# Performance work log

Measured on AMD Instinct MI355X. Metric: run time of the kernel, lower is better.

Reference implementation:

```python
import jax, jax.numpy as jnp
import numpy as np

E = 256

def setup_inputs() -> dict:
    key = jax.random.key(0)
    ks = jax.random.split(key, 10)
    N, T_y, T_x = 8, 300, 160
    s = 1.0 / np.sqrt(E)  # torch-style uniform-ish init scale, keeps gates unsaturated
    return {
        "inputs": jax.random.normal(ks[0], (N, T_y, E // 2), jnp.float32),
        "memory": jax.random.normal(ks[1], (N, T_x, E), jnp.float32),
        "h0": jnp.zeros((1, N, E), jnp.float32),
        "Wih": jax.random.normal(ks[2], (3 * E, E // 2), jnp.float32) * s,
        "Whh": jax.random.normal(ks[3], (3 * E, E), jnp.float32) * s,
        "bih": jax.random.normal(ks[4], (3 * E,), jnp.float32) * s,
        "bhh": jax.random.normal(ks[5], (3 * E,), jnp.float32) * s,
        "W": jax.random.normal(ks[6], (E, E), jnp.float32) * s,
        "U": jax.random.normal(ks[7], (E, E), jnp.float32) * s,
        "v": jax.random.normal(ks[8], (E,), jnp.float32) * s,
    }


def reference(inputs, memory, h0, Wih, Whh, bih, bhh, W, U, v):
    # GRU (PyTorch gate order r, z, n), batch_first, single layer, unidirectional.
    def step(h, x_t):
        gi = x_t @ Wih.T + bih      # [N, 3E]
        gh = h @ Whh.T + bhh        # [N, 3E]
        ir, iz, i_n = jnp.split(gi, 3, axis=-1)
        hr, hz, hn = jnp.split(gh, 3, axis=-1)
        r = jax.nn.sigmoid(ir + hr)
        z = jax.nn.sigmoid(iz + hz)
        n = jnp.tanh(i_n + r * hn)
        h_new = (1.0 - z) * n + z * h
        return h_new, h_new

    h_last, outs = jax.lax.scan(step, h0[0], jnp.swapaxes(inputs, 0, 1))
    outputs = jnp.swapaxes(outs, 0, 1)   # [N, T_y, E]
    hidden = h_last[None]                # [1, N, E]

    # Bahdanau additive attention
    w = outputs @ W.T                    # [N, T_y, E]
    u = memory @ U.T                     # [N, T_x, E]
    # scores: v . tanh(w + u) broadcast over [N, T_y, T_x, E]
    scores = jnp.einsum('ntxe,e->ntx', jnp.tanh(w[:, :, None, :] + u[:, None, :, :]), v)
    attn_weights = jax.nn.softmax(scores, axis=2)  # [N, T_y, T_x]
    return attn_weights, outputs, hidden
```

## Files before the change

### kernel.cpp

```cpp
#include <hip/hip_runtime.h>


typedef _Float16 f16x2 __attribute__((ext_vector_type(2)));
typedef _Float16 f16x8 __attribute__((ext_vector_type(8)));
typedef float f32x4 __attribute__((ext_vector_type(4)));

__device__ __forceinline__ float fexp2(float x) { return __builtin_amdgcn_exp2f(x); }
__device__ __forceinline__ float frcp(float x) { return __builtin_amdgcn_rcpf(x); }
__device__ __forceinline__ float fsig(float x) {
    return frcp(1.0f + fexp2(x * -1.4426950408889634f));
}
__device__ __forceinline__ float ftanh(float x) {
    return 1.0f - 2.0f * frcp(1.0f + fexp2(x * 2.8853900817779268f));
}

__device__ __forceinline__ float pick4(f32x4 v, int s) {
    float ab = (s & 1) ? v[1] : v[0];
    float cd = (s & 1) ? v[3] : v[2];
    return (s & 2) ? cd : ab;
}

#define FLAG(i) ((i) * 32)

__global__ __launch_bounds__(256) void phase1_kernel(
    const float* __restrict__ Whh, unsigned* __restrict__ wd,
    const float* __restrict__ inputs, const float* __restrict__ Wih,
    float* __restrict__ gi, const float* __restrict__ bih,
    const float* __restrict__ bhh) {
    if (blockIdx.x < 384) {
        int gid = blockIdx.x * 256 + threadIdx.x;
        int i = gid >> 9, t = gid & 511;
        int fi = i >> 2, j = i & 3;
        int g = fi >> 4, m2 = (fi >> 3) & 1, ks = fi & 7;
        int w = t >> 6, l = t & 63;
        int row = 256 * g + 32 * w + 16 * m2 + (l & 15);
        int k = 32 * ks + 8 * (l >> 4) + 2 * j;
        union { unsigned u; f16x2 h; } cv;
        cv.h[0] = (_Float16)Whh[(size_t)row * 256 + k];
        cv.h[1] = (_Float16)Whh[(size_t)row * 256 + k + 1];
        wd[i * 512 + t] = cv.u;
        return;
    }
    int id = blockIdx.x - 384;
    const int n0 = (id % 12) * 64, m0 = (id / 12) * 64;
    __shared__ float Xs[32][65];
    __shared__ float Ws2[32][65];
    const int tid = threadIdx.x;
    const int tx = tid & 15, ty = tid >> 4;
    const int M = 2400, K = 128;
    float acc[4][4] = {};
    for (int k0 = 0; k0 < K; k0 += 32) {
#pragma unroll
        for (int i = 0; i < 8; ++i) {
            int e = tid + i * 256;
            int kk = e & 31, m = e >> 5;
            int row = m0 + m;
            Xs[kk][m] = (row < M) ? inputs[(size_t)row * K + k0 + kk] : 0.0f;
            Ws2[kk][m] = Wih[(size_t)(n0 + m) * K + k0 + kk];
        }
        __syncthreads();
#pragma unroll
        for (int kk = 0; kk < 32; ++kk) {
            float a[4], b[4];
#pragma unroll
            for (int i = 0; i < 4; ++i) a[i] = Xs[kk][ty * 4 + i];
#pragma unroll
            for (int j = 0; j < 4; ++j) b[j] = Ws2[kk][tx * 4 + j];
#pragma unroll
            for (int i = 0; i < 4; ++i)
#pragma unroll
                for (int j = 0; j < 4; ++j) acc[i][j] += a[i] * b[j];
        }
        __syncthreads();
    }
#pragma unroll
    for (int i = 0; i < 4; ++i) {
        int row = m0 + ty * 4 + i;
        if (row >= M) continue;
        int b = row / 300;
        int t = row - b * 300;
#pragma unroll
        for (int j = 0; j < 4; ++j) {
            int col = n0 + tx * 4 + j;
            float val = acc[i][j] + ((col < 512) ? (bih[col] + bhh[col]) : bih[col]);
            gi[(size_t)(t * 8 + b) * 768 + col] = val;
        }
    }
}

__global__ __launch_bounds__(256) void gemm_kernel(
    const float* __restrict__ X, const float* __restrict__ Wt,
    float* __restrict__ C, _Float16* __restrict__ C16,
    int M, int N, int K, int mode) {
    __shared__ float Xs[32][65];
    __shared__ float Ws2[32][65];
    const int n0 = blockIdx.x * 64, m0 = blockIdx.y * 64;
    const int tid = threadIdx.x;
    const int tx = tid & 15, ty = tid >> 4;
    float acc[4][4] = {};
    for (int k0 = 0; k0 < K; k0 += 32) {
#pragma unroll
        for (int i = 0; i < 8; ++i) {
            int e = tid + i * 256;
            int kk = e & 31, m = e >> 5;
            int row = m0 + m;
            Xs[kk][m] = (row < M) ? X[(size_t)row * K + k0 + kk] : 0.0f;
            Ws2[kk][m] = Wt[(size_t)(n0 + m) * K + k0 + kk];
        }
        __syncthreads();
#pragma unroll
        for (int kk = 0; kk < 32; ++kk) {
            float a[4], b[4];
#pragma unroll
            for (int i = 0; i < 4; ++i) a[i] = Xs[kk][ty * 4 + i];
#pragma unroll
            for (int j = 0; j < 4; ++j) b[j] = Ws2[kk][tx * 4 + j];
#pragma unroll
            for (int i = 0; i < 4; ++i)
#pragma unroll
                for (int j = 0; j < 4; ++j) acc[i][j] += a[i] * b[j];
        }
        __syncthreads();
    }
#pragma unroll
    for (int i = 0; i < 4; ++i) {
        int row = m0 + ty * 4 + i;
        if (row >= M) continue;
#pragma unroll
        for (int j = 0; j < 4; ++j) {
            int col = n0 + tx * 4 + j;
            if (mode == 2) C16[(size_t)row * N + col] = (_Float16)acc[i][j];
            else           C[(size_t)row * N + col] = acc[i][j];
        }
    }
}

__global__ __launch_bounds__(512, 1) void gru_mega(
    float* __restrict__ gi, unsigned* __restrict__ wd,
    const float* __restrict__ h0, const float* __restrict__ bhh,
    float* __restrict__ outs, float* __restrict__ hid,
    const float* __restrict__ memory, const float* __restrict__ Um,
    _Float16* __restrict__ u16, const float* __restrict__ W,
    const float* __restrict__ vv, float* __restrict__ attn,
    const float* __restrict__ Whh, const float* __restrict__ inputs,
    const float* __restrict__ Wih, const float* __restrict__ bih,
    int* flags, int full) {
    __shared__ __align__(16) _Float16 hbuf[2][256];
    __shared__ float Xs[32][65];
    __shared__ float Ws2[32][65];
    __shared__ unsigned uS[160 * 129];
    __shared__ __align__(16) float oL[10][260];
    __shared__ float wLf[10][256];
    __shared__ float vL[256];
    __shared__ float scP[2][2][160];
    __shared__ float sc2[2][160];
    __shared__ float red2[2][2];

    const int tid = threadIdx.x;

    if (full) {
        for (int task = blockIdx.x; task < 840; task += 248) {
            if (task < 384) {
                if (tid < 256) {
                    int gid = task * 256 + tid;
                    int i = gid >> 9, t = gid & 511;
                    int fi = i >> 2, j = i & 3;
                    int g = fi >> 4, m2 = (fi >> 3) & 1, ks = fi & 7;
                    int w = t >> 6, l = t & 63;
                    int row = 256 * g + 32 * w + 16 * m2 + (l & 15);
                    int k = 32 * ks + 8 * (l >> 4) + 2 * j;
                    union { unsigned u; f16x2 h; } cv;
                    cv.h[0] = (_Float16)Whh[(size_t)row * 256 + k];
                    cv.h[1] = (_Float16)Whh[(size_t)row * 256 + k + 1];
                    wd[i * 512 + t] = cv.u;
                }
            } else {
                int tt = task - 384;
                const int n0 = (tt % 12) * 64, m0 = (tt / 12) * 64;
                const int tx = tid & 15, ty = tid >> 4;
                float acc[2][4] = {};
                for (int k0 = 0; k0 < 128; k0 += 32) {
#pragma unroll
                    for (int i = 0; i < 4; ++i) {
                        int e = tid + i * 512;
                        int kk = e & 31, m = e >> 5;
                        int row = m0 + m;
                        Xs[kk][m] = (row < 2400)
                                        ? inputs[(size_t)row * 128 + k0 + kk]
                                        : 0.0f;
                        Ws2[kk][m] = Wih[(size_t)(n0 + m) * 128 + k0 + kk];
                    }
                    __syncthreads();
#pragma unroll
                    for (int kk = 0; kk < 32; ++kk) {
                        float a0 = Xs[kk][ty * 2], a1 = Xs[kk][ty * 2 + 1];
                        float b0 = Ws2[kk][tx * 4 + 0];
                        float b1 = Ws2[kk][tx * 4 + 1];
                        float b2 = Ws2[kk][tx * 4 + 2];
                        float b3 = Ws2[kk][tx * 4 + 3];
                        acc[0][0] += a0 * b0; acc[0][1] += a0 * b1;
                        acc[0][2] += a0 * b2; acc[0][3] += a0 * b3;
                        acc[1][0] += a1 * b0; acc[1][1] += a1 * b1;
                        acc[1][2] += a1 * b2; acc[1][3] += a1 * b3;
                    }
                    __syncthreads();
                }
#pragma unroll
                for (int i = 0; i < 2; ++i) {
                    int row = m0 + ty * 2 + i;
                    if (row < 2400) {
                        int bb = row / 300;
                        int t2 = row - bb * 300;
#pragma unroll
                        for (int j = 0; j < 4; ++j) {
                            int col = n0 + tx * 4 + j;
                            float val = acc[i][j] +
                                ((col < 512) ? (bih[col] + bhh[col]) : bih[col]);
                            gi[(size_t)(t2 * 8 + bb) * 768 + col] = val;
                        }
                    }
                }
            }
            __syncthreads();
        }
        asm volatile("s_waitcnt vmcnt(0)" ::: "memory");
        __syncthreads();
        if (tid == 0) {
            __hip_atomic_fetch_add(&flags[FLAG(9)], 1, __ATOMIC_RELEASE,
                                   __HIP_MEMORY_SCOPE_AGENT);
            while (__hip_atomic_load(&flags[FLAG(9)], __ATOMIC_ACQUIRE,
                                     __HIP_MEMORY_SCOPE_AGENT) < 248)
                __builtin_amdgcn_s_sleep(16);
        }
        __syncthreads();
    }

    if (blockIdx.x >= 8) {
        int id = blockIdx.x - 8;
        if (id < 80) {
            const int n0 = (id & 3) * 64, m0 = (id >> 2) * 64;
            const int tx = tid & 15, ty = (tid & 255) >> 4;
            float acc[4][4] = {};
            for (int k0 = 0; k0 < 256; k0 += 32) {
                if (tid < 256) {
#pragma unroll
                    for (int i = 0; i < 8; ++i) {
                        int e = tid + i * 256;
                        int kk = e & 31, m = e >> 5;
                        Xs[kk][m] = memory[(size_t)(m0 + m) * 256 + k0 + kk];
                        Ws2[kk][m] = Um[(size_t)(n0 + m) * 256 + k0 + kk];
                    }
                }
                __syncthreads();
                if (tid < 256) {
#pragma unroll
                    for (int kk = 0; kk < 32; ++kk) {
                        float a[4], b[4];
#pragma unroll
                        for (int i = 0; i < 4; ++i) a[i] = Xs[kk][ty * 4 + i];
#pragma unroll
                        for (int j = 0; j < 4; ++j) b[j] = Ws2[kk][tx * 4 + j];
#pragma unroll
                        for (int i = 0; i < 4; ++i)
#pragma unroll
                            for (int j = 0; j < 4; ++j) acc[i][j] += a[i] * b[j];
                    }
                }
                __syncthreads();
            }
            if (tid < 256) {
#pragma unroll
                for (int i = 0; i < 4; ++i)
#pragma unroll
                    for (int j = 0; j < 4; ++j)
                        u16[(size_t)(m0 + ty * 4 + i) * 256 + n0 + tx * 4 + j] =
                            (_Float16)acc[i][j];
            }
            if (!full) return;
            __syncthreads();
            if (tid == 0)
                __hip_atomic_fetch_add(&flags[FLAG(8)], 1, __ATOMIC_RELEASE,
                                       __HIP_MEMORY_SCOPE_AGENT);
        }
        if (!full) return;

        const int grp = id / 30;
        const int tc = id % 30;
        if (tid == 0) {
            while (__hip_atomic_load(&flags[FLAG(8)], __ATOMIC_RELAXED,
                                     __HIP_MEMORY_SCOPE_AGENT) < 80)
                __builtin_amdgcn_s_sleep(64);
            while (__hip_atomic_load(&flags[FLAG(8)], __ATOMIC_ACQUIRE,
                                     __HIP_MEMORY_SCOPE_AGENT) < 80)
                __builtin_amdgcn_s_sleep(8);
        }
        __syncthreads();
        const unsigned* ug = (const unsigned*)(u16 + (size_t)grp * 160 * 256);
        for (int i = tid; i < 20480; i += 512)
            uS[(i >> 7) * 129 + (i & 127)] = ug[i];
        if (tid < 256) vL[tid] = vv[tid];
        __syncthreads();

        if (tid == 0) {
            while (__hip_atomic_load(&flags[FLAG(grp)], __ATOMIC_RELAXED,
                                     __HIP_MEMORY_SCOPE_AGENT) < 1)
                __builtin_amdgcn_s_sleep(127);
            while (__hip_atomic_load(&flags[FLAG(grp)], __ATOMIC_ACQUIRE,
                                     __HIP_MEMORY_SCOPE_AGENT) < 1)
                __builtin_amdgcn_s_sleep(8);
        }
        __syncthreads();
        for (int i = tid; i < 2560; i += 512) {
            int ti = i >> 8, k = i & 255;
            oL[ti][k] = outs[((size_t)grp * 300 + tc * 10 + ti) * 256 + k];
        }
        __syncthreads();
        {
            const int c = tid & 255, rh = tid >> 8;
            float a0 = 0, a1 = 0, a2 = 0, a3 = 0, a4 = 0;
            const float* wr = W + (size_t)c * 256;
            const int r0 = rh * 5;
            for (int k4 = 0; k4 < 256; k4 += 4) {
                float4 wq = *(const float4*)(wr + k4);
#define WROW(ACC, TI)                                                     \
                {                                                         \
                    float4 oq = *(const float4*)(&oL[TI][k4]);            \
                    ACC += wq.x * oq.x + wq.y * oq.y +                    \
                           wq.z * oq.z + wq.w * oq.w;                     \
                }
                WROW(a0, r0 + 0) WROW(a1, r0 + 1) WROW(a2, r0 + 2)
                WROW(a3, r0 + 3) WROW(a4, r0 + 4)
#undef WROW
            }
            wLf[r0 + 0][c] = a0; wLf[r0 + 1][c] = a1; wLf[r0 + 2][c] = a2;
            wLf[r0 + 3][c] = a3; wLf[r0 + 4][c] = a4;
        }
        __syncthreads();
        for (int tp = 0; tp < 5; ++tp) {
            const int ti0 = tp * 2;
            if (tid < 320) {
                const int x = (tid < 160) ? tid : tid - 160;
                const int half = (tid >= 160) ? 1 : 0;
                const unsigned* ur = uS + x * 129 + half * 64;
                const float* wl0 = wLf[ti0] + half * 128;
                const float* wl1 = wLf[ti0 + 1] + half * 128;
                const float* vl = vL + half * 128;
                float a0 = 0.f, b0 = 0.f, a1 = 0.f, b1 = 0.f;
#pragma unroll 8
                for (int e2 = 0; e2 < 64; ++e2) {
                    union { unsigned uu2; _Float16 hh[2]; } cv;
                    cv.uu2 = ur[e2];
                    int ee = e2 * 2;
                    float u0 = (float)cv.hh[0], u1 = (float)cv.hh[1];
                    float v0 = vl[ee], v1 = vl[ee + 1];
                    a0 += v0 * ftanh(wl0[ee] + u0);
                    b0 += v1 * ftanh(wl0[ee + 1] + u1);
                    a1 += v0 * ftanh(wl1[ee] + u0);
                    b1 += v1 * ftanh(wl1[ee + 1] + u1);
                }
                scP[0][half][x] = a0 + b0;
                scP[1][half][x] = a1 + b1;
            }
            __syncthreads();
            if (tid < 320) {
                int r = (tid >= 160) ? 1 : 0;
                int x = r ? tid - 160 : tid;
                sc2[r][x] = scP[r][0][x] + scP[r][1][x];
            }
            __syncthreads();
            if (tid < 128) {
                int r = tid >> 6, lane = tid & 63;
                float m = -3.0e38f;
                for (int i = lane; i < 160; i += 64) m = fmaxf(m, sc2[r][i]);
#pragma unroll
                for (int o = 32; o; o >>= 1) m = fmaxf(m, __shfl_xor(m, o));
                if (lane == 0) red2[r][0] = m;
            }
            __syncthreads();
            if (tid < 320) {
                int r = (tid >= 160) ? 1 : 0;
                int x = r ? tid - 160 : tid;
                sc2[r][x] = fexp2((sc2[r][x] - red2[r][0]) *
                                  1.4426950408889634f);
            }
            __syncthreads();
            if (tid < 128) {
                int r = tid >> 6, lane = tid & 63;
                float s = 0.0f;
                for (int i = lane; i < 160; i += 64) s += sc2[r][i];
#pragma unroll
                for (int o = 32; o; o >>= 1) s += __shfl_xor(s, o);
                if (lane == 0) red2[r][1] = s;
            }
            __syncthreads();
            if (tid < 320) {
                int r = (tid >= 160) ? 1 : 0;
                int x = r ? tid - 160 : tid;
                attn[(size_t)(grp * 300 + tc * 10 + ti0 + r) * 160 + x] =
                    sc2[r][x] * frcp(red2[r][1]);
            }
            __syncthreads();
        }
        return;
    }

    const int b = blockIdx.x;
    const int t = tid;
    const int w = t >> 6, l = t & 63;
    const int grp = l >> 4;
    const int sel = l & 7;
    const int hi = (l >> 3) & 1;
    const int m2s = sel >> 2, rsel = sel & 3;
    const int e = 32 * w + 16 * m2s + 4 * grp + rsel;

    f16x8 wf[48];
#pragma unroll
    for (int fi = 0; fi < 48; ++fi) {
        union { unsigned u[4]; f16x8 v; } cv;
#pragma unroll
        for (int j = 0; j < 4; ++j) cv.u[j] = wd[(fi * 4 + j) * 512 + t];
        wf[fi] = cv.v;
    }

    float h = h0[b * 256 + e];
    float bn = bhh[512 + e];
    if (!hi) hbuf[0][e] = (_Float16)h;
    const float* gp = gi + b * 768;
    float* op = outs + (size_t)b * 76800 + e;

    float gr = gp[e], gz = gp[e + 256], gn = gp[e + 512];
    __syncthreads();

    for (int st = 0; st < 300; ++st) {
        int stn = (st < 299) ? st + 1 : st;
        const float* g = gp + (size_t)stn * 6144;
        float grn = g[e], gzn = g[e + 256], gnn = g[e + 512];

        const _Float16* hb = hbuf[st & 1];
        f16x8 hv0 = *(const f16x8*)(hb + 0 * 32 + 8 * grp);
        f16x8 hv1 = *(const f16x8*)(hb + 1 * 32 + 8 * grp);
        f16x8 hv2 = *(const f16x8*)(hb + 2 * 32 + 8 * grp);
        f16x8 hv3 = *(const f16x8*)(hb + 3 * 32 + 8 * grp);
        f16x8 hv4 = *(const f16x8*)(hb + 4 * 32 + 8 * grp);
        f16x8 hv5 = *(const f16x8*)(hb + 5 * 32 + 8 * grp);
        f16x8 hv6 = *(const f16x8*)(hb + 6 * 32 + 8 * grp);
        f16x8 hv7 = *(const f16x8*)(hb + 7 * 32 + 8 * grp);

        f32x4 aR0 = {0.f, 0.f, 0.f, 0.f}, aR1 = {0.f, 0.f, 0.f, 0.f};
        f32x4 aZ0 = {0.f, 0.f, 0.f, 0.f}, aZ1 = {0.f, 0.f, 0.f, 0.f};
        f32x4 aN0 = {0.f, 0.f, 0.f, 0.f}, aN1 = {0.f, 0.f, 0.f, 0.f};
#define KSTEP(ks, hv)                                                        \
        aR0 = __builtin_amdgcn_mfma_f32_16x16x32_f16(wf[0 * 8 + ks], hv, aR0, 0, 0, 0); \
        aR1 = __builtin_amdgcn_mfma_f32_16x16x32_f16(wf[1 * 8 + ks], hv, aR1, 0, 0, 0); \
        aZ0 = __builtin_amdgcn_mfma_f32_16x16x32_f16(wf[2 * 8 + ks], hv, aZ0, 0, 0, 0); \
        aZ1 = __builtin_amdgcn_mfma_f32_16x16x32_f16(wf[3 * 8 + ks], hv, aZ1, 0, 0, 0); \
        aN0 = __builtin_amdgcn_mfma_f32_16x16x32_f16(wf[4 * 8 + ks], hv, aN0, 0, 0, 0); \
        aN1 = __builtin_amdgcn_mfma_f32_16x16x32_f16(wf[5 * 8 + ks], hv, aN1, 0, 0, 0);
        KSTEP(0, hv0) KSTEP(1, hv1) KSTEP(2, hv2) KSTEP(3, hv3)
        KSTEP(4, hv4) KSTEP(5, hv5) KSTEP(6, hv6) KSTEP(7, hv7)
#undef KSTEP

        f32x4 vR = m2s ? aR1 : aR0;
        f32x4 vZ = m2s ? aZ1 : aZ0;
        f32x4 vN = m2s ? aN1 : aN0;
        float sr = pick4(vR, rsel);
        float sz = pick4(vZ, rsel);
        float sn = pick4(vN, rsel);

        float r = fsig(gr + sr);
        float z = fsig(gz + sz);
        float n = ftanh(gn + r * (sn + bn));
        h = n + z * (h - n);

        gr = grn; gz = gzn; gn = gnn;

        if (hi)
            op[st * 256] = h;
        else
            hbuf[(st + 1) & 1][e] = (_Float16)h;
        asm volatile("s_waitcnt lgkmcnt(0)\n\ts_barrier" ::: "memory");
    }
    if (!hi) hid[b * 256 + e] = h;
    if (full) {
        asm volatile("s_waitcnt vmcnt(0)" ::: "memory");
        __syncthreads();
        if (t == 0)
            __hip_atomic_store(&flags[FLAG(b)], 1, __ATOMIC_RELEASE,
                               __HIP_MEMORY_SCOPE_AGENT);
    }
}

__global__ __launch_bounds__(256) void wattn_kernel(
    const _Float16* __restrict__ u16, const float* __restrict__ outs,
    const float* __restrict__ W, const float* __restrict__ vv,
    float* __restrict__ attn) {
    const int tc = blockIdx.x, b = blockIdx.y;
    const int tid = threadIdx.x;
    __shared__ unsigned uS[160 * 129];
    __shared__ __align__(16) float oL[10][260];
    __shared__ float wLf[10][256];
    __shared__ float vL[256], sc[160], red[2];

    const unsigned* ug = (const unsigned*)(u16 + (size_t)b * 160 * 256);
    for (int i = tid; i < 20480; i += 256)
        uS[(i >> 7) * 129 + (i & 127)] = ug[i];
    vL[tid] = vv[tid];
    for (int i = tid; i < 2560; i += 256) {
        int ti = i >> 8, k = i & 255;
        oL[ti][k] = outs[((size_t)b * 300 + tc * 10 + ti) * 256 + k];
    }
    __syncthreads();
    {
        float a0 = 0, a1 = 0, a2 = 0, a3 = 0, a4 = 0;
        float a5 = 0, a6 = 0, a7 = 0, a8 = 0, a9 = 0;
        for (int k4 = 0; k4 < 256; k4 += 4) {
            float4 wq = *(const float4*)(W + (size_t)tid * 256 + k4);
#define WROW(ACC, TI)                                                     \
            {                                                             \
                float4 oq = *(const float4*)(&oL[TI][k4]);                \
                ACC += wq.x * oq.x + wq.y * oq.y +                        \
                       wq.z * oq.z + wq.w * oq.w;                        \
            }
            WROW(a0, 0) WROW(a1, 1) WROW(a2, 2) WROW(a3, 3) WROW(a4, 4)
            WROW(a5, 5) WROW(a6, 6) WROW(a7, 7) WROW(a8, 8) WROW(a9, 9)
#undef WROW
        }
        wLf[0][tid] = a0; wLf[1][tid] = a1; wLf[2][tid] = a2;
        wLf[3][tid] = a3; wLf[4][tid] = a4; wLf[5][tid] = a5;
        wLf[6][tid] = a6; wLf[7][tid] = a7; wLf[8][tid] = a8;
        wLf[9][tid] = a9;
    }
    __syncthreads();
    for (int ti = 0; ti < 10; ++ti) {
        int t = tc * 10 + ti;
        float acc2 = 0.0f;
        if (tid < 160) {
            const unsigned* ur = uS + tid * 129;
            const float* wl = wLf[ti];
#pragma unroll 8
            for (int e2 = 0; e2 < 128; ++e2) {
                union { unsigned uu2; _Float16 hh[2]; } cv;
                cv.uu2 = ur[e2];
                int ee = e2 * 2;
                acc2 += vL[ee] * ftanh(wl[ee] + (float)cv.hh[0]);
                acc2 += vL[ee + 1] * ftanh(wl[ee + 1] + (float)cv.hh[1]);
            }
            sc[tid] = acc2;
        }
        __syncthreads();
        if (tid < 64) {
            float m = -3.0e38f;
            for (int i = tid; i < 160; i += 64) m = fmaxf(m, sc[i]);
#pragma unroll
            for (int o = 32; o; o >>= 1) m = fmaxf(m, __shfl_xor(m, o));
            if (tid == 0) red[0] = m;
        }
        __syncthreads();
        float ee = 0.0f;
        if (tid < 160) {
            ee = fexp2((acc2 - red[0]) * 1.4426950408889634f);
            sc[tid] = ee;
        }
        __syncthreads();
        if (tid < 64) {
            float s = 0.0f;
            for (int i = tid; i < 160; i += 64) s += sc[i];
#pragma unroll
            for (int o = 32; o; o >>= 1) s += __shfl_xor(s, o);
            if (tid == 0) red[1] = s;
        }
        __syncthreads();
        if (tid < 160)
            attn[(size_t)(b * 300 + t) * 160 + tid] = ee * frcp(red[1]);
        __syncthreads();
    }
}

extern "C" void kernel_launch(void* const* d_in, const int* in_sizes, int n_in,
                              void* d_out, int out_size, void* d_ws, size_t ws_size,
                              hipStream_t stream) {
    const float* inputs = (const float*)d_in[0];
    const float* memory = (const float*)d_in[1];
    const float* h0 = (const float*)d_in[2];
    const float* Wih = (const float*)d_in[3];
    const float* Whh = (const float*)d_in[4];
    const float* bih = (const float*)d_in[5];
    const float* bhh = (const float*)d_in[6];
    const float* Wm = (const float*)d_in[7];
    const float* Um = (const float*)d_in[8];
    const float* vv = (const float*)d_in[9];

    float* out = (float*)d_out;
    float* out_attn = out;
    float* out_outputs = out + 384000;
    float* out_hidden = out + 998400;

    char* ws = (char*)d_ws;
    float* gi = (float*)ws;
    unsigned* wd = (unsigned*)(ws + 7372800);

    const size_t U16_OFF = 7766016, FLAG_OFF = 8421376;
    const bool full = ws_size >= FLAG_OFF + 1280;
    _Float16* u16 = full ? (_Float16*)(ws + U16_OFF) : (_Float16*)ws;
    int* flags = (int*)(ws + FLAG_OFF);

    if (full) {
        hipMemsetAsync(flags, 0, 1280, stream);
        gru_mega<<<248, 512, 0, stream>>>(gi, wd, h0, bhh, out_outputs,
                                          out_hidden, memory, Um, u16, Wm, vv,
                                          out_attn, Whh, inputs, Wih, bih,
                                          flags, 1);
    } else {
        phase1_kernel<<<840, 256, 0, stream>>>(Whh, wd, inputs, Wih, gi, bih,
                                               bhh);
        gru_mega<<<8, 512, 0, stream>>>(gi, wd, h0, bhh, out_outputs,
                                        out_hidden, memory, Um, u16, Wm, vv,
                                        out_attn, Whh, inputs, Wih, bih,
                                        flags, 0);
        gemm_kernel<<<dim3(4, 20), 256, 0, stream>>>(memory, Um, nullptr, u16,
                                                     1280, 256, 256, 2);
        wattn_kernel<<<dim3(30, 8), 256, 0, stream>>>(u16, out_outputs, Wm, vv,
                                                      out_attn);
    }
}
```

Before: 484.1 us.

## Replace grid-wide barrier with one-way flag so GRU blocks alone wait for precompute

The 8 recurrence blocks no longer take part in the precompute work. The grid-wide barrier is replaced: the other 240 blocks signal a counter, and only the GRU blocks wait on it before loading weights. The other blocks can then go straight on to the memory@U.T GEMM without waiting for everyone. The input-projection GEMM tile grows from a 2x4 to a 4x4 microtile per thread, computed by 256 threads. Flag polling is split into a relaxed system-scope peek followed by one acquire load, and some sleep intervals are changed. This risks memory-ordering subtleties from mixing system and agent scopes.

```diff
diff --git a/kernel.cpp b/kernel.cpp
--- a/kernel.cpp
+++ b/kernel.cpp
@@ -21,6 +21,13 @@
 }
 
 #define FLAG(i) ((i) * 32)
+
+__device__ __forceinline__ int flag_peek(int* p) {
+    return __hip_atomic_load(p, __ATOMIC_RELAXED, __HIP_MEMORY_SCOPE_SYSTEM);
+}
+__device__ __forceinline__ void flag_fence(int* p) {
+    (void)__hip_atomic_load(p, __ATOMIC_ACQUIRE, __HIP_MEMORY_SCOPE_AGENT);
+}
 
 __global__ __launch_bounds__(256) void phase1_kernel(
     const float* __restrict__ Whh, unsigned* __restrict__ wd,
@@ -158,85 +165,88 @@
 
     const int tid = threadIdx.x;
 
-    if (full) {
-        for (int task = blockIdx.x; task < 840; task += 248) {
-            if (task < 384) {
-                if (tid < 256) {
-                    int gid = task * 256 + tid;
-                    int i = gid >> 9, t = gid & 511;
-                    int fi = i >> 2, j = i & 3;
-                    int g = fi >> 4, m2 = (fi >> 3) & 1, ks = fi & 7;
-                    int w = t >> 6, l = t & 63;
-                    int row = 256 * g + 32 * w + 16 * m2 + (l & 15);
-                    int k = 32 * ks + 8 * (l >> 4) + 2 * j;
-                    union { unsigned u; f16x2 h; } cv;
-                    cv.h[0] = (_Float16)Whh[(size_t)row * 256 + k];
-                    cv.h[1] = (_Float16)Whh[(size_t)row * 256 + k + 1];
-                    wd[i * 512 + t] = cv.u;
-                }
-            } else {
-                int tt = task - 384;
-                const int n0 = (tt % 12) * 64, m0 = (tt / 12) * 64;
-                const int tx = tid & 15, ty = tid >> 4;
-                float acc[2][4] = {};
-                for (int k0 = 0; k0 < 128; k0 += 32) {
-#pragma unroll
-                    for (int i = 0; i < 4; ++i) {
-                        int e = tid + i * 512;
-                        int kk = e & 31, m = e >> 5;
-                        int row = m0 + m;
-                        Xs[kk][m] = (row < 2400)
-                                        ? inputs[(size_t)row * 128 + k0 + kk]
-                                        : 0.0f;
-                        Ws2[kk][m] = Wih[(size_t)(n0 + m) * 128 + k0 + kk];
+    if (blockIdx.x >= 8) {
+        int id = blockIdx.x - 8;
+        if (full) {
+            for (int task = id; task < 840; task += 240) {
+                if (task < 384) {
+                    if (tid < 256) {
+                        int gid = task * 256 + tid;
+                        int i = gid >> 9, t = gid & 511;
+                        int fi = i >> 2, j = i & 3;
+                        int g = fi >> 4, m2 = (fi >> 3) & 1, ks = fi & 7;
+                        int w = t >> 6, l = t & 63;
+                        int row = 256 * g + 32 * w + 16 * m2 + (l & 15);
+                        int k = 32 * ks + 8 * (l >> 4) + 2 * j;
+                        union { unsigned u; f16x2 h; } cv;
+                        cv.h[0] = (_Float16)Whh[(size_t)row * 256 + k];
+                        cv.h[1] = (_Float16)Whh[(size_t)row * 256 + k + 1];
+                        wd[i * 512 + t] = cv.u;
                     }
-                    __syncthreads();
-#pragma unroll
-                    for (int kk = 0; kk < 32; ++kk) {
-                        float a0 = Xs[kk][ty * 2], a1 = Xs[kk][ty * 2 + 1];
-                        float b0 = Ws2[kk][tx * 4 + 0];
-                        float b1 = Ws2[kk][tx * 4 + 1];
-                        float b2 = Ws2[kk][tx * 4 + 2];
-                        float b3 = Ws2[kk][tx * 4 + 3];
-                        acc[0][0] += a0 * b0; acc[0][1] += a0 * b1;
-                        acc[0][2] += a0 * b2; acc[0][3] += a0 * b3;
-                        acc[1][0] += a1 * b0; acc[1][1] += a1 * b1;
-                        acc[1][2] += a1 * b2; acc[1][3] += a1 * b3;
+                } else {
+                    int tt = task - 384;
+                    const int n0 = (tt % 12) * 64, m0 = (tt / 12) * 64;
+                    const int tx = tid & 15, ty = tid >> 4;
+                    float acc[4][4] = {};
+                    for (int k0 = 0; k0 < 128; k0 += 32) {
+                        if (tid < 256) {
+#pragma unroll
+                            for (int i = 0; i < 8; ++i) {
+                                int e = tid + i * 256;
+                                int kk = e & 31, m = e >> 5;
+                                int row = m0 + m;
+                                Xs[kk][m] = (row < 2400)
+                                    ? inputs[(size_t)row * 128 + k0 + kk]
+                                    : 0.0f;
+                                Ws2[kk][m] =
+                                    Wih[(size_t)(n0 + m) * 128 + k0 + kk];
+                            }
+                        }
+                        __syncthreads();
+                        if (tid < 256) {
+#pragma unroll
+                            for (int kk = 0; kk < 32; ++kk) {
+                                float a[4], b[4];
+#pragma unroll
+                                for (int i = 0; i < 4; ++i)
+                                    a[i] = Xs[kk][ty * 4 + i];
+#pragma unroll
+                                for (int j = 0; j < 4; ++j)
+                                    b[j] = Ws2[kk][tx * 4 + j];
+#pragma unroll
+                                for (int i = 0; i < 4; ++i)
+#pragma unroll
+                                    for (int j = 0; j < 4; ++j)
+                                        acc[i][j] += a[i] * b[j];
+                            }
+                        }
+                        __syncthreads();
                     }
-                    __syncthreads();
-                }
-#pragma unroll
-                for (int i = 0; i < 2; ++i) {
-                    int row = m0 + ty * 2 + i;
-                    if (row < 2400) {
-                        int bb = row / 300;
-                        int t2 = row - bb * 300;
-#pragma unroll
-                        for (int j = 0; j < 4; ++j) {
-                            int col = n0 + tx * 4 + j;
-                            float val = acc[i][j] +
-                                ((col < 512) ? (bih[col] + bhh[col]) : bih[col]);
-                            gi[(size_t)(t2 * 8 + bb) * 768 + col] = val;
+                    if (tid < 256) {
+#pragma unroll
+                        for (int i = 0; i < 4; ++i) {
+                            int row = m0 + ty * 4 + i;
+                            if (row >= 2400) continue;
+                            int bb = row / 300;
+                            int t2 = row - bb * 300;
+#pragma unroll
+                            for (int j = 0; j < 4; ++j) {
+                                int col = n0 + tx * 4 + j;
+                                float val = acc[i][j] +
+                                    ((col < 512) ? (bih[col] + bhh[col])
+                                                 : bih[col]);
+                                gi[(size_t)(t2 * 8 + bb) * 768 + col] = val;
+                            }
                         }
                     }
                 }
             }
-            __syncthreads();
-        }
-        asm volatile("s_waitcnt vmcnt(0)" ::: "memory");
-        __syncthreads();
-        if (tid == 0) {
-            __hip_atomic_fetch_add(&flags[FLAG(9)], 1, __ATOMIC_RELEASE,
-                                   __HIP_MEMORY_SCOPE_AGENT);
-            while (__hip_atomic_load(&flags[FLAG(9)], __ATOMIC_ACQUIRE,
-                                     __HIP_MEMORY_SCOPE_AGENT) < 248)
-                __builtin_amdgcn_s_sleep(16);
-        }
-        __syncthreads();
-    }
-
-    if (blockIdx.x >= 8) {
-        int id = blockIdx.x - 8;
+            asm volatile("s_waitcnt vmcnt(0)" ::: "memory");
+            __syncthreads();
+            if (tid == 0)
+                __hip_atomic_fetch_add(&flags[FLAG(9)], 1, __ATOMIC_RELEASE,
+                                       __HIP_MEMORY_SCOPE_AGENT);
+        }
         if (id < 80) {
             const int n0 = (id & 3) * 64, m0 = (id >> 2) * 64;
             const int tx = tid & 15, ty = (tid & 255) >> 4;
@@ -280,19 +290,16 @@
             __syncthreads();
             if (tid == 0)
                 __hip_atomic_fetch_add(&flags[FLAG(8)], 1, __ATOMIC_RELEASE,
-                                       __HIP_MEMORY_SCOPE_AGENT);
+                                       __HIP_MEMORY_SCOPE_SYSTEM);
         }
         if (!full) return;
 
         const int grp = id / 30;
         const int tc = id % 30;
         if (tid == 0) {
-            while (__hip_atomic_load(&flags[FLAG(8)], __ATOMIC_RELAXED,
-                                     __HIP_MEMORY_SCOPE_AGENT) < 80)
+            while (flag_peek(&flags[FLAG(8)]) < 80)
                 __builtin_amdgcn_s_sleep(64);
-            while (__hip_atomic_load(&flags[FLAG(8)], __ATOMIC_ACQUIRE,
-                                     __HIP_MEMORY_SCOPE_AGENT) < 80)
-                __builtin_amdgcn_s_sleep(8);
+            flag_fence(&flags[FLAG(8)]);
         }
         __syncthreads();
         const unsigned* ug = (const unsigned*)(u16 + (size_t)grp * 160 * 256);
@@ -302,12 +309,9 @@
         __syncthreads();
 
         if (tid == 0) {
-            while (__hip_atomic_load(&flags[FLAG(grp)], __ATOMIC_RELAXED,
-                                     __HIP_MEMORY_SCOPE_AGENT) < 1)
-                __builtin_amdgcn_s_sleep(127);
-            while (__hip_atomic_load(&flags[FLAG(grp)], __ATOMIC_ACQUIRE,
-                                     __HIP_MEMORY_SCOPE_AGENT) < 1)
-                __builtin_amdgcn_s_sleep(8);
+            while (flag_peek(&flags[FLAG(grp)]) < 1)
+                __builtin_amdgcn_s_sleep(96);
+            flag_fence(&flags[FLAG(grp)]);
         }
         __syncthreads();
         for (int i = tid; i < 2560; i += 512) {
@@ -413,6 +417,15 @@
     const int m2s = sel >> 2, rsel = sel & 3;
     const int e = 32 * w + 16 * m2s + 4 * grp + rsel;
 
+    if (full) {
+        if (t == 0) {
+            while (flag_peek(&flags[FLAG(9)]) < 240)
+                __builtin_amdgcn_s_sleep(16);
+            flag_fence(&flags[FLAG(9)]);
+        }
+        __syncthreads();
+    }
+
     f16x8 wf[48];
 #pragma unroll
     for (int fi = 0; fi < 48; ++fi) {
@@ -486,7 +499,7 @@
         __syncthreads();
         if (t == 0)
             __hip_atomic_store(&flags[FLAG(b)], 1, __ATOMIC_RELEASE,
-                               __HIP_MEMORY_SCOPE_AGENT);
+                               __HIP_MEMORY_SCOPE_SYSTEM);
     }
 }
 
```

New measurement: 471.5 us. 2.6% less time.
